# Kernel tuning notes

Measured on AMD Instinct MI355X. Metric: run time of the kernel, lower is better.

Reference implementation:

```python
import jax, jax.numpy as jnp
import numpy as np

TEMPERATURE = 0.5
BATCH = 2048  # N = batch_size * world_size (world_size = 1)
FEAT = 128
EPS = 1e-8  # torch CosineSimilarity default eps


def _build_mask_indices(N):
    """Replicates mask_correlated_samples + the row-major boolean gather
    sim[mask].reshape(2N, -1). Returns static flat indices [2N, 2N-1]."""
    sub = np.ones((2 * N, 2 * N), dtype=bool)
    np.fill_diagonal(sub, False)
    idx = np.arange(N)
    sub[idx, N + idx] = False
    sub[N + idx, idx] = False
    mask = np.zeros((3 * N, 3 * N), dtype=bool)
    mask[:2 * N, :2 * N] = sub
    mask[idx, 2 * N + idx] = True
    mask[2 * N + idx, idx] = True
    flat = np.nonzero(mask.ravel())[0]  # row-major order, 2N*(2N-1) entries
    return flat.reshape(2 * N, 2 * N - 1)


_NEG_IDX = jnp.asarray(_build_mask_indices(BATCH), dtype=jnp.int32)


def setup_inputs() -> dict:
    key = jax.random.key(0)
    ka, kp, kn = jax.random.split(key, 3)
    return {
        "anchor": jax.random.normal(ka, (BATCH, FEAT), dtype=jnp.float32),
        "pos": jax.random.normal(kp, (BATCH, FEAT), dtype=jnp.float32),
        "neg": jax.random.normal(kn, (BATCH, FEAT), dtype=jnp.float32),
    }


def reference(anchor, pos, neg):
    N = anchor.shape[0]
    z = jnp.concatenate([anchor, pos, neg], axis=0)  # [3N, d]
    zn = z / jnp.maximum(jnp.linalg.norm(z, axis=1, keepdims=True), EPS)
    sim = (zn @ zn.T) / TEMPERATURE  # [3N, 3N]
    # positive pairs: diagonals at offset +/-2N (anchor<->neg pairs)
    sim_i_j = jnp.diagonal(sim, offset=2 * N)[:N]
    sim_j_i = jnp.diagonal(sim, offset=-2 * N)[:N]
    positive = jnp.concatenate([sim_i_j, sim_j_i]).reshape(2 * N, 1)
    # masked gather of negatives (static index table, row-major order)
    negative = jnp.take(sim.ravel(), _NEG_IDX)  # [2N, 2N-1]
    logits = jnp.concatenate([positive, negative], axis=1)  # [2N, 2N]
    # cross-entropy with label 0, reduction='sum', then / (2N)
    loss = jnp.sum(jax.nn.logsumexp(logits, axis=1) - logits[:, 0]) / (2 * N)
    return loss
```

## Files before the change

kernel.cpp:

```cpp
#include <hip/hip_runtime.h>
#include <hip/hip_bf16.h>

#define N_      2048
#define TWO_N   4096
#define DFEAT   128
#define SCALE   2.0f
#define BROWS   128
#define BCOLS   128
#define NT      (BCOLS / 16)
#define LDSTR   132

typedef __attribute__((ext_vector_type(8))) short bf16x8;
typedef __attribute__((ext_vector_type(4))) float f32x4;

__global__ __launch_bounds__(256) void k_prep(const float* __restrict__ a,
                                              const float* __restrict__ p,
                                              const float* __restrict__ ng,
                                              __hip_bfloat16* __restrict__ zn16,
                                              float* __restrict__ dvec,
                                              float* __restrict__ accS,
                                              float* __restrict__ accP) {
  const int wave = threadIdx.x >> 6;
  const int lane = threadIdx.x & 63;
  const int row  = blockIdx.x * 4 + wave;

  if (threadIdx.x < 4)        accS[blockIdx.x * 4 + threadIdx.x] = 0.0f;
  else if (threadIdx.x < 6)   accP[blockIdx.x * 2 + threadIdx.x - 4] = 0.0f;

  if (row < N_) {
    float2 u = ((const float2*)(a  + (size_t)row * DFEAT))[lane];
    float2 w = ((const float2*)(ng + (size_t)row * DFEAT))[lane];
    float saa = u.x * u.x + u.y * u.y;
    float snn = w.x * w.x + w.y * w.y;
    float san = u.x * w.x + u.y * w.y;
#pragma unroll
    for (int m = 1; m < 64; m <<= 1) {
      saa += __shfl_xor(saa, m);
      snn += __shfl_xor(snn, m);
      san += __shfl_xor(san, m);
    }
    float na = fmaxf(sqrtf(saa), 1e-8f);
    float rn = 1.0f / na;
    __hip_bfloat162 h;
    h.x = __float2bfloat16(u.x * rn);
    h.y = __float2bfloat16(u.y * rn);
    ((__hip_bfloat162*)zn16)[row * (DFEAT / 2) + lane] = h;
    if (lane == 0)
      dvec[row] = SCALE * san / (na * fmaxf(sqrtf(snn), 1e-8f));
  } else {
    float2 v = ((const float2*)(p + (size_t)(row - N_) * DFEAT))[lane];
    float ss = v.x * v.x + v.y * v.y;
#pragma unroll
    for (int m = 1; m < 64; m <<= 1) ss += __shfl_xor(ss, m);
    float rn = 1.0f / fmaxf(sqrtf(ss), 1e-8f);
    __hip_bfloat162 h;
    h.x = __float2bfloat16(v.x * rn);
    h.y = __float2bfloat16(v.y * rn);
    ((__hip_bfloat162*)zn16)[row * (DFEAT / 2) + lane] = h;
  }
}

__global__ __launch_bounds__(256) void k_simsum(const __hip_bfloat16* __restrict__ zn16,
                                                float* __restrict__ accS,
                                                float* __restrict__ accP) {
  __shared__ __align__(16) short Bp[BCOLS * LDSTR];

  const int wave = threadIdx.x >> 6;
  const int lane = threadIdx.x & 63;
  const int lr   = lane & 15;
  const int kg   = lane >> 4;
  const int rows_base = blockIdx.x * BROWS + wave * 32;
  const int cb0 = blockIdx.y * BCOLS;
  const short* zs = (const short*)zn16;

  bf16x8 a0[4], a1[4];
#pragma unroll
  for (int kk = 0; kk < 4; ++kk) {
    a0[kk] = *(const bf16x8*)(zs + (size_t)(rows_base + lr) * DFEAT + kk * 32 + kg * 8);
    a1[kk] = *(const bf16x8*)(zs + (size_t)(rows_base + 16 + lr) * DFEAT + kk * 32 + kg * 8);
  }

#pragma unroll
  for (int it = 0; it < 8; ++it) {
    const int g   = it * 256 + threadIdx.x;
    const int col = g >> 4;
    const int q   = g & 15;
    bf16x8 v = *(const bf16x8*)(zs + (size_t)(cb0 + col) * DFEAT + q * 8);
    *(bf16x8*)(&Bp[col * LDSTR + q * 8]) = v;
  }
  __syncthreads();

  const bool hi = (rows_base >= N_);
  int rrow[2][4], prt[2][4];
#pragma unroll
  for (int t = 0; t < 2; ++t)
#pragma unroll
    for (int j = 0; j < 4; ++j) {
      rrow[t][j] = rows_base + t * 16 + kg * 4 + j;
      prt[t][j]  = hi ? (rrow[t][j] - N_) : (rrow[t][j] + N_);
    }

  float accPv[2][4] = {{0.f,0.f,0.f,0.f},{0.f,0.f,0.f,0.f}};
  float accSv[2][4] = {{0.f,0.f,0.f,0.f},{0.f,0.f,0.f,0.f}};

  bf16x8 bcur[4], bnxt[4];
#pragma unroll
  for (int kk = 0; kk < 4; ++kk)
    bcur[kk] = *(const bf16x8*)(&Bp[lr * LDSTR + kk * 32 + kg * 8]);

#pragma unroll 2
  for (int ct = 0; ct < NT; ++ct) {
    const int ctn = (ct + 1 < NT) ? (ct + 1) : ct;
#pragma unroll
    for (int kk = 0; kk < 4; ++kk)
      bnxt[kk] = *(const bf16x8*)(&Bp[(ctn * 16 + lr) * LDSTR + kk * 32 + kg * 8]);

    f32x4 acc0 = {0.f, 0.f, 0.f, 0.f};
    f32x4 acc1 = {0.f, 0.f, 0.f, 0.f};
#pragma unroll
    for (int kk = 0; kk < 4; ++kk) {
      acc0 = __builtin_amdgcn_mfma_f32_16x16x32_bf16(a0[kk], bcur[kk], acc0, 0, 0, 0);
      acc1 = __builtin_amdgcn_mfma_f32_16x16x32_bf16(a1[kk], bcur[kk], acc1, 0, 0, 0);
    }

    const int c = cb0 + ct * 16 + lr;
#pragma unroll
    for (int j = 0; j < 4; ++j) {
      {
        float e = __expf(SCALE * acc0[j]);
        const bool excl = (c == rrow[0][j]) || (c == prt[0][j]);
        e = excl ? 0.0f : e;
        if (hi) {
          const bool toP = (c < prt[0][j]);
          accPv[0][j] += toP ? e : 0.0f;
          accSv[0][j] += toP ? 0.0f : e;
        } else {
          accSv[0][j] += e;
        }
      }
      {
        float e = __expf(SCALE * acc1[j]);
        const bool excl = (c == rrow[1][j]) || (c == prt[1][j]);
        e = excl ? 0.0f : e;
        if (hi) {
          const bool toP = (c < prt[1][j]);
          accPv[1][j] += toP ? e : 0.0f;
          accSv[1][j] += toP ? 0.0f : e;
        } else {
          accSv[1][j] += e;
        }
      }
    }

#pragma unroll
    for (int kk = 0; kk < 4; ++kk) bcur[kk] = bnxt[kk];
  }

#pragma unroll
  for (int t = 0; t < 2; ++t)
#pragma unroll
    for (int j = 0; j < 4; ++j) {
      float pv = accPv[t][j], sv = accSv[t][j];
#pragma unroll
      for (int m = 1; m < 16; m <<= 1) {
        sv += __shfl_xor(sv, m);
        if (hi) pv += __shfl_xor(pv, m);
      }
      if (lr == 0) {
        atomicAdd(&accS[rrow[t][j]], sv);
        if (hi) atomicAdd(&accP[rrow[t][j] - N_], pv);
      }
    }
}

__global__ __launch_bounds__(1024) void k_final(const float* __restrict__ dvec,
                                                const float* __restrict__ accS,
                                                const float* __restrict__ accP,
                                                float* __restrict__ out) {
  __shared__ float Elds[N_];
  __shared__ float red[16];
  const int tid = threadIdx.x;
  float dpart = 0.f;
  for (int i = tid; i < N_; i += 1024) {
    float E = __expf(dvec[i]);
    Elds[i] = E;
    dpart += E;
  }
#pragma unroll
  for (int m = 1; m < 64; m <<= 1) dpart += __shfl_xor(dpart, m);
  const int w = tid >> 6, l = tid & 63;
  if (l == 0) red[w] = dpart;
  __syncthreads();
  float Dsum = 0.f;
#pragma unroll
  for (int k = 0; k < 16; ++k) Dsum += red[k];
  __syncthreads();

  float part = 0.f;
  for (int r = tid; r < TWO_N; r += 1024) {
    float S = accS[r];
    float t;
    if (r < N_) {
      t = logf(2.0f * Elds[r] + S) - dvec[r];
    } else {
      const int i = r - N_;
      const float extra = (i < N_ - 1) ? accP[i + 1] : Dsum;
      t = logf(Elds[i] + S + extra) - dvec[i];
    }
    part += t;
  }
#pragma unroll
  for (int m = 1; m < 64; m <<= 1) part += __shfl_xor(part, m);
  if (l == 0) red[w] = part;
  __syncthreads();
  if (tid == 0) {
    float tot = 0.f;
#pragma unroll
    for (int k = 0; k < 16; ++k) tot += red[k];
    out[0] = tot / (float)TWO_N;
  }
}

extern "C" void kernel_launch(void* const* d_in, const int* in_sizes, int n_in,
                              void* d_out, int out_size, void* d_ws, size_t ws_size,
                              hipStream_t stream) {
  const float* a  = (const float*)d_in[0];
  const float* p  = (const float*)d_in[1];
  const float* ng = (const float*)d_in[2];

  char* ws = (char*)d_ws;
  __hip_bfloat16* zn16 = (__hip_bfloat16*)ws;
  float* dvec = (float*)(ws + (size_t)TWO_N * DFEAT * 2);
  float* accS = dvec + TWO_N;
  float* accP = accS + TWO_N;

  k_prep<<<TWO_N / 4, 256, 0, stream>>>(a, p, ng, zn16, dvec, accS, accP);
  k_simsum<<<dim3(TWO_N / BROWS, TWO_N / BCOLS), 256, 0, stream>>>(zn16, accS, accP);
  k_final<<<1, 1024, 0, stream>>>(dvec, accS, accP, (float*)d_out);
}
```

Measured before the change: 25.28 us.

## Fuse final reduction into simsum via last-block counter; specialize tile exclusion logic

Removes the separate single-block final kernel by having the last-finishing simsum block (detected through an atomic counter reset in prep) compute the loss. Also classifies each tile by its position relative to the diagonal and positive-pair offsets, so most tiles run a plain exp-sum loop without per-element mask and compare logic. This saves one kernel launch and shortens the inner epilogue. In exchange it adds a global atomic and fences per block, and the final reduction now runs on only 256 threads.

After: 100.2 us. +296.5%, slower.

```diff
diff --git a/kernel.cpp b/kernel.cpp
--- a/kernel.cpp
+++ b/kernel.cpp
@@ -9,6 +9,7 @@
 #define BCOLS   128
 #define NT      (BCOLS / 16)
 #define LDSTR   132
+#define NBLK    1024
 
 typedef __attribute__((ext_vector_type(8))) short bf16x8;
 typedef __attribute__((ext_vector_type(4))) float f32x4;
@@ -19,13 +20,15 @@
                                               __hip_bfloat16* __restrict__ zn16,
                                               float* __restrict__ dvec,
                                               float* __restrict__ accS,
-                                              float* __restrict__ accP) {
+                                              float* __restrict__ accP,
+                                              unsigned int* __restrict__ counter) {
   const int wave = threadIdx.x >> 6;
   const int lane = threadIdx.x & 63;
   const int row  = blockIdx.x * 4 + wave;
 
   if (threadIdx.x < 4)        accS[blockIdx.x * 4 + threadIdx.x] = 0.0f;
   else if (threadIdx.x < 6)   accP[blockIdx.x * 2 + threadIdx.x - 4] = 0.0f;
+  if (blockIdx.x == 0 && threadIdx.x == 6) counter[0] = 0u;
 
   if (row < N_) {
     float2 u = ((const float2*)(a  + (size_t)row * DFEAT))[lane];
@@ -61,17 +64,30 @@
 }
 
 __global__ __launch_bounds__(256) void k_simsum(const __hip_bfloat16* __restrict__ zn16,
+                                                const float* __restrict__ dvec,
                                                 float* __restrict__ accS,
-                                                float* __restrict__ accP) {
+                                                float* __restrict__ accP,
+                                                unsigned int* __restrict__ counter,
+                                                float* __restrict__ out) {
   __shared__ __align__(16) short Bp[BCOLS * LDSTR];
-
+  __shared__ float red[4];
+  __shared__ unsigned int slast;
+
+  const int bx = blockIdx.x, by = blockIdx.y;
   const int wave = threadIdx.x >> 6;
   const int lane = threadIdx.x & 63;
   const int lr   = lane & 15;
   const int kg   = lane >> 4;
-  const int rows_base = blockIdx.x * BROWS + wave * 32;
-  const int cb0 = blockIdx.y * BCOLS;
+  const int rows_base = bx * BROWS + wave * 32;
+  const int cb0 = by * BCOLS;
   const short* zs = (const short*)zn16;
+
+  const bool hi = (bx >= 16);
+  const int cls = (by == bx) ? 0
+                : (!hi && by == bx + 16) ? 1
+                : (hi && by == bx - 16) ? 2
+                : (hi && by < bx - 16) ? 3
+                : 4;
 
   bf16x8 a0[4], a1[4];
 #pragma unroll
@@ -90,18 +106,19 @@
   }
   __syncthreads();
 
-  const bool hi = (rows_base >= N_);
-  int rrow[2][4], prt[2][4];
+  int rrow[2][4], excl[2][4];
 #pragma unroll
   for (int t = 0; t < 2; ++t)
 #pragma unroll
     for (int j = 0; j < 4; ++j) {
       rrow[t][j] = rows_base + t * 16 + kg * 4 + j;
-      prt[t][j]  = hi ? (rrow[t][j] - N_) : (rrow[t][j] + N_);
-    }
-
-  float accPv[2][4] = {{0.f,0.f,0.f,0.f},{0.f,0.f,0.f,0.f}};
-  float accSv[2][4] = {{0.f,0.f,0.f,0.f},{0.f,0.f,0.f,0.f}};
+      excl[t][j] = (cls == 0) ? rrow[t][j]
+                 : (cls == 1) ? rrow[t][j] + N_
+                 : (cls == 2) ? rrow[t][j] - N_ : -1;
+    }
+
+  float acc1v[2][4] = {{0.f,0.f,0.f,0.f},{0.f,0.f,0.f,0.f}};
+  float acc2v[2][4] = {{0.f,0.f,0.f,0.f},{0.f,0.f,0.f,0.f}};
 
   bf16x8 bcur[4], bnxt[4];
 #pragma unroll
@@ -124,101 +141,92 @@
     }
 
     const int c = cb0 + ct * 16 + lr;
+    if (cls == 4 || cls == 3) {
+#pragma unroll
+      for (int j = 0; j < 4; ++j) {
+        acc1v[0][j] += __expf(SCALE * acc0[j]);
+        acc1v[1][j] += __expf(SCALE * acc1[j]);
+      }
+    } else if (cls == 2) {
+#pragma unroll
+      for (int j = 0; j < 4; ++j) {
+        float e0 = __expf(SCALE * acc0[j]);
+        e0 = (c == excl[0][j]) ? 0.0f : e0;
+        if (c < excl[0][j]) acc2v[0][j] += e0; else acc1v[0][j] += e0;
+        float e1 = __expf(SCALE * acc1[j]);
+        e1 = (c == excl[1][j]) ? 0.0f : e1;
+        if (c < excl[1][j]) acc2v[1][j] += e1; else acc1v[1][j] += e1;
+      }
+    } else {
+#pragma unroll
+      for (int j = 0; j < 4; ++j) {
+        float e0 = __expf(SCALE * acc0[j]);
+        acc1v[0][j] += (c == excl[0][j]) ? 0.0f : e0;
+        float e1 = __expf(SCALE * acc1[j]);
+        acc1v[1][j] += (c == excl[1][j]) ? 0.0f : e1;
+      }
+    }
+
+#pragma unroll
+    for (int kk = 0; kk < 4; ++kk) bcur[kk] = bnxt[kk];
+  }
+
+#pragma unroll
+  for (int t = 0; t < 2; ++t)
 #pragma unroll
     for (int j = 0; j < 4; ++j) {
-      {
-        float e = __expf(SCALE * acc0[j]);
-        const bool excl = (c == rrow[0][j]) || (c == prt[0][j]);
-        e = excl ? 0.0f : e;
-        if (hi) {
-          const bool toP = (c < prt[0][j]);
-          accPv[0][j] += toP ? e : 0.0f;
-          accSv[0][j] += toP ? 0.0f : e;
-        } else {
-          accSv[0][j] += e;
-        }
-      }
-      {
-        float e = __expf(SCALE * acc1[j]);
-        const bool excl = (c == rrow[1][j]) || (c == prt[1][j]);
-        e = excl ? 0.0f : e;
-        if (hi) {
-          const bool toP = (c < prt[1][j]);
-          accPv[1][j] += toP ? e : 0.0f;
-          accSv[1][j] += toP ? 0.0f : e;
-        } else {
-          accSv[1][j] += e;
-        }
-      }
-    }
-
-#pragma unroll
-    for (int kk = 0; kk < 4; ++kk) bcur[kk] = bnxt[kk];
-  }
-
-#pragma unroll
-  for (int t = 0; t < 2; ++t)
-#pragma unroll
-    for (int j = 0; j < 4; ++j) {
-      float pv = accPv[t][j], sv = accSv[t][j];
+      float v1 = acc1v[t][j], v2 = acc2v[t][j];
 #pragma unroll
       for (int m = 1; m < 16; m <<= 1) {
-        sv += __shfl_xor(sv, m);
-        if (hi) pv += __shfl_xor(pv, m);
+        v1 += __shfl_xor(v1, m);
+        if (cls == 2) v2 += __shfl_xor(v2, m);
       }
       if (lr == 0) {
-        atomicAdd(&accS[rrow[t][j]], sv);
-        if (hi) atomicAdd(&accP[rrow[t][j] - N_], pv);
-      }
-    }
-}
-
-__global__ __launch_bounds__(1024) void k_final(const float* __restrict__ dvec,
-                                                const float* __restrict__ accS,
-                                                const float* __restrict__ accP,
-                                                float* __restrict__ out) {
-  __shared__ float Elds[N_];
-  __shared__ float red[16];
+        const int r = rrow[t][j];
+        if (cls == 3)      atomicAdd(&accP[r - N_], v1);
+        else               atomicAdd(&accS[r], v1);
+        if (cls == 2)      atomicAdd(&accP[r - N_], v2);
+      }
+    }
+
+  __threadfence();
+  __syncthreads();
+  if (threadIdx.x == 0)
+    slast = __hip_atomic_fetch_add(counter, 1u, __ATOMIC_ACQ_REL,
+                                   __HIP_MEMORY_SCOPE_AGENT);
+  __syncthreads();
+  if (slast != NBLK - 1) return;
+  __threadfence();
+
   const int tid = threadIdx.x;
   float dpart = 0.f;
-  for (int i = tid; i < N_; i += 1024) {
-    float E = __expf(dvec[i]);
-    Elds[i] = E;
-    dpart += E;
-  }
+  for (int i = tid; i < N_; i += 256) dpart += __expf(dvec[i]);
 #pragma unroll
   for (int m = 1; m < 64; m <<= 1) dpart += __shfl_xor(dpart, m);
-  const int w = tid >> 6, l = tid & 63;
-  if (l == 0) red[w] = dpart;
-  __syncthreads();
-  float Dsum = 0.f;
-#pragma unroll
-  for (int k = 0; k < 16; ++k) Dsum += red[k];
+  if (lane == 0) red[wave] = dpart;
+  __syncthreads();
+  const float Dsum = red[0] + red[1] + red[2] + red[3];
   __syncthreads();
 
   float part = 0.f;
-  for (int r = tid; r < TWO_N; r += 1024) {
+  for (int r = tid; r < TWO_N; r += 256) {
     float S = accS[r];
-    float t;
+    float v;
     if (r < N_) {
-      t = logf(2.0f * Elds[r] + S) - dvec[r];
+      v = logf(2.0f * __expf(dvec[r]) + S) - dvec[r];
     } else {
       const int i = r - N_;
       const float extra = (i < N_ - 1) ? accP[i + 1] : Dsum;
-      t = logf(Elds[i] + S + extra) - dvec[i];
-    }
-    part += t;
+      v = logf(__expf(dvec[i]) + S + extra) - dvec[i];
+    }
+    part += v;
   }
 #pragma unroll
   for (int m = 1; m < 64; m <<= 1) part += __shfl_xor(part, m);
-  if (l == 0) red[w] = part;
-  __syncthreads();
-  if (tid == 0) {
-    float tot = 0.f;
-#pragma unroll
-    for (int k = 0; k < 16; ++k) tot += red[k];
-    out[0] = tot / (float)TWO_N;
-  }
+  if (lane == 0) red[wave] = part;
+  __syncthreads();
+  if (tid == 0)
+    out[0] = (red[0] + red[1] + red[2] + red[3]) / (float)TWO_N;
 }
 
 extern "C" void kernel_launch(void* const* d_in, const int* in_sizes, int n_in,
@@ -233,8 +241,9 @@
   float* dvec = (float*)(ws + (size_t)TWO_N * DFEAT * 2);
   float* accS = dvec + TWO_N;
   float* accP = accS + TWO_N;
-
-  k_prep<<<TWO_N / 4, 256, 0, stream>>>(a, p, ng, zn16, dvec, accS, accP);
-  k_simsum<<<dim3(TWO_N / BROWS, TWO_N / BCOLS), 256, 0, stream>>>(zn16, accS, accP);
-  k_final<<<1, 1024, 0, stream>>>(dvec, accS, accP, (float*)d_out);
+  unsigned int* counter = (unsigned int*)(accP + N_);
+
+  k_prep<<<TWO_N / 4, 256, 0, stream>>>(a, p, ng, zn16, dvec, accS, accP, counter);
+  k_simsum<<<dim3(TWO_N / BROWS, TWO_N / BCOLS), 256, 0, stream>>>(
+      zn16, dvec, accS, accP, counter, (float*)d_out);
 }
```
